# Kernel optimization log

Hardware: AMD Instinct MI355X
Metric: run time of the kernel (lower is better)

## Reference

```python
import jax, jax.numpy as jnp
import numpy as np

DIM = 384
WH, WW = 7, 7
N_HEADS = 12
HEAD_DIM = DIM // N_HEADS
SCALE = HEAD_DIM ** -0.5


def _relative_position_index(Wh, Ww):
    coords = np.stack(np.meshgrid(np.arange(Wh), np.arange(Ww), indexing='ij'))  # (2,Wh,Ww)
    cf = coords.reshape(2, -1)                       # (2, N)
    rc = cf[:, :, None] - cf[:, None, :]             # (2, N, N)
    rc = rc.transpose(1, 2, 0).copy()                # (N, N, 2)
    rc[..., 0] += Wh - 1
    rc[..., 1] += Ww - 1
    rc[..., 0] *= 2 * Ww - 1
    return jnp.asarray(rc.sum(-1))                   # (N, N) int

REL_IDX = _relative_position_index(WH, WW)


def setup_inputs() -> dict:
    key = jax.random.key(0)
    ks = jax.random.split(key, 5)
    B_, N, C = 4096, WH * WW, DIM
    nW = 64
    x = jax.random.normal(ks[0], (B_, N, C), dtype=jnp.float32)
    mask = jnp.zeros((nW, N, N), dtype=jnp.float32)  # 0/-inf additive mask; zeros = no shift
    qkv_w = jax.random.normal(ks[1], (3 * C, C), dtype=jnp.float32) * (C ** -0.5)
    qkv_b = jnp.zeros((3 * C,), dtype=jnp.float32)
    proj_w = jax.random.normal(ks[2], (C, C), dtype=jnp.float32) * (C ** -0.5)
    proj_b = jnp.zeros((C,), dtype=jnp.float32)
    rpb_table = jax.random.normal(ks[3], ((2 * WH - 1) * (2 * WW - 1), N_HEADS), dtype=jnp.float32) * 0.02
    return {"x": x, "mask": mask, "qkv_w": qkv_w, "qkv_b": qkv_b,
            "proj_w": proj_w, "proj_b": proj_b, "rpb_table": rpb_table}


def reference(x, mask, qkv_w, qkv_b, proj_w, proj_b, rpb_table):
    B_, N, C = x.shape
    H, hd = N_HEADS, HEAD_DIM
    # qkv projection -> (3, B_, H, N, hd)
    qkv = (x @ qkv_w.T + qkv_b).reshape(B_, N, 3, H, hd).transpose(2, 0, 3, 1, 4)
    q, k, v = qkv[0] * SCALE, qkv[1], qkv[2]
    attn = jnp.einsum('bhnd,bhmd->bhnm', q, k)                       # (B_, H, N, N)
    rpb = rpb_table[REL_IDX.reshape(-1)].reshape(N, N, H).transpose(2, 0, 1)  # (H, N, N)
    attn = attn + rpb[None]
    nW = mask.shape[0]
    attn = attn.reshape(B_ // nW, nW, H, N, N) + mask[None, :, None]
    attn = attn.reshape(B_, H, N, N)
    attn = jax.nn.softmax(attn, axis=-1)
    out = jnp.einsum('bhnm,bhmd->bhnd', attn, v)                     # (B_, H, N, hd)
    out = out.transpose(0, 2, 1, 3).reshape(B_, N, C)
    return out @ proj_w.T + proj_b
```

## Files before the change

### kernel.cpp

```cpp
#include <hip/hip_runtime.h>
#include <stdint.h>


typedef unsigned short u16;
typedef short short8 __attribute__((ext_vector_type(8)));
typedef float f32x4 __attribute__((ext_vector_type(4)));

static __device__ __forceinline__ u16 f2bf(float f) {
  unsigned u = __builtin_bit_cast(unsigned, f);
  return (u16)((u + 0x7fffu + ((u >> 16) & 1u)) >> 16);
}

static __device__ __forceinline__ void async_cp16(const u16* g, u16* l) {
  __builtin_amdgcn_global_load_lds(
      (__attribute__((address_space(1))) unsigned int*)g,
      (__attribute__((address_space(3))) unsigned int*)l, 16, 0, 0);
}

__global__ __launch_bounds__(256) void prep_kernel(
    const float* __restrict__ x, const float* __restrict__ wq,
    const float* __restrict__ wp, const float* __restrict__ rpt,
    u16* __restrict__ xb, u16* __restrict__ wqb, u16* __restrict__ wpb,
    float* __restrict__ rpbf)
{
  const int bid = blockIdx.x, tid = threadIdx.x;
  if (bid < 1024) {
    const float4* x4 = (const float4*)x;
    ushort4* o4 = (ushort4*)xb;
    for (unsigned i = bid * 256u + tid; i < 19267584u; i += 262144u) {
      float4 v = x4[i];
      ushort4 o; o.x = f2bf(v.x); o.y = f2bf(v.y); o.z = f2bf(v.z); o.w = f2bf(v.w);
      o4[i] = o;
    }
  } else if (bid < 1088) {
    for (unsigned i = (bid - 1024) * 256u + tid; i < 147456u; i += 16384u) {
      if (i < 110592u) {
        float4 v = ((const float4*)wq)[i];
        ushort4 o; o.x = f2bf(v.x); o.y = f2bf(v.y); o.z = f2bf(v.z); o.w = f2bf(v.w);
        ((ushort4*)wqb)[i] = o;
      } else {
        unsigned k = i - 110592u;
        float4 v = ((const float4*)wp)[k];
        ushort4 o; o.x = f2bf(v.x); o.y = f2bf(v.y); o.z = f2bf(v.z); o.w = f2bf(v.w);
        ((ushort4*)wpb)[k] = o;
      }
    }
  } else {
    for (int e = (bid - 1088) * 256 + tid; e < 28812; e += 2048) {
      int h = e / 2401, r2 = e - h * 2401;
      int i = r2 / 49, j = r2 - (r2 / 49) * 49;
      int rel = (i / 7 - j / 7 + 6) * 13 + (i % 7 - j % 7 + 6);
      rpbf[e] = rpt[rel * 12 + h];
    }
  }
}

template <int MODE>
__global__ __launch_bounds__(256) void gemm_nt(
    const u16* __restrict__ A, const u16* __restrict__ Bw,
    const float* __restrict__ bias, void* __restrict__ Cp, int Ntot)
{
  __shared__ u16 As[128 * 32];
  __shared__ u16 Bs[128 * 32];
  const int tid = threadIdx.x;
  const int wave = tid >> 6, lane = tid & 63;
  const int lr = lane & 15, quad = lane >> 4;
  const int m0 = blockIdx.y * 128, n0 = blockIdx.x * 128;
  const int wm = (wave & 1) * 64, wn = (wave >> 1) * 64;

  const int e0 = tid * 8;
  const int row0 = e0 >> 5, col0 = e0 & 31;

  f32x4 acc[4][4] = {};
  for (int k0 = 0; k0 < 384; k0 += 32) {
    __syncthreads();
    async_cp16(&A[(size_t)(m0 + row0) * 384 + k0 + col0],      As + wave * 512);
    async_cp16(&A[(size_t)(m0 + 64 + row0) * 384 + k0 + col0], As + 2048 + wave * 512);
    async_cp16(&Bw[(size_t)(n0 + row0) * 384 + k0 + col0],      Bs + wave * 512);
    async_cp16(&Bw[(size_t)(n0 + 64 + row0) * 384 + k0 + col0], Bs + 2048 + wave * 512);
    __syncthreads();

    short8 af[4], bf[4];
#pragma unroll
    for (int mi = 0; mi < 4; ++mi)
      af[mi] = *(const short8*)&As[(wm + mi * 16 + lr) * 32 + quad * 8];
#pragma unroll
    for (int ni = 0; ni < 4; ++ni)
      bf[ni] = *(const short8*)&Bs[(wn + ni * 16 + lr) * 32 + quad * 8];
#pragma unroll
    for (int mi = 0; mi < 4; ++mi)
#pragma unroll
      for (int ni = 0; ni < 4; ++ni)
        acc[mi][ni] = __builtin_amdgcn_mfma_f32_16x16x32_bf16(af[mi], bf[ni], acc[mi][ni], 0, 0, 0);
  }

  float bv[4];
#pragma unroll
  for (int ni = 0; ni < 4; ++ni) bv[ni] = bias[n0 + wn + ni * 16 + lr];
#pragma unroll
  for (int mi = 0; mi < 4; ++mi)
#pragma unroll
    for (int ni = 0; ni < 4; ++ni) {
      const int gcol = n0 + wn + ni * 16 + lr;
#pragma unroll
      for (int r = 0; r < 4; ++r) {
        const size_t grow = (size_t)(m0 + wm + mi * 16 + quad * 4 + r);
        float v = acc[mi][ni][r] + bv[ni];
        if (MODE == 0) {
          if (gcol < 384) v *= 0.17677669529663687f;
          ((u16*)Cp)[grow * Ntot + gcol] = f2bf(v);
        } else {
          ((float*)Cp)[grow * Ntot + gcol] = v;
        }
      }
    }
}

__global__ __launch_bounds__(256) void attn_kernel(
    const u16* __restrict__ qkv, const float* __restrict__ mask,
    const float* __restrict__ rpbf, u16* __restrict__ attnout)
{
  __shared__ u16 P_lds[4][64 * 64];
  __shared__ u16 VT_lds[4][32 * 64];
  const int tid = threadIdx.x;
  const int wave = tid >> 6, lane = tid & 63;
  const int lr = lane & 15, quad = lane >> 4;
  const int b = blockIdx.x / 3;
  const int h = (blockIdx.x - b * 3) * 4 + wave;

  const size_t base = (size_t)b * (49 * 1152);
  u16* P  = P_lds[wave];
  u16* Vt = VT_lds[wave];
  const short8 z8 = {0, 0, 0, 0, 0, 0, 0, 0};

  {
    const int dh = lane & 3;
    const int tk0 = lane >> 2;
#pragma unroll
    for (int p = 0; p < 4; ++p) {
      const int tok = p * 16 + tk0;
      short8 v = z8;
      if (tok < 49)
        v = *(const short8*)&qkv[base + (size_t)tok * 1152 + 768 + h * 32 + dh * 8];
#pragma unroll
      for (int j = 0; j < 8; ++j) {
        const int d = dh * 8 + j;
        Vt[d * 64 + (((tok >> 3) ^ j) * 8) + (tok & 7)] = ((const u16*)&v)[j];
      }
    }
  }

  short8 qf[4], kf[4];
#pragma unroll
  for (int mi = 0; mi < 4; ++mi) {
    const int row = mi * 16 + lr;
    qf[mi] = (row < 49)
        ? *(const short8*)&qkv[base + (size_t)row * 1152 + h * 32 + quad * 8] : z8;
  }
#pragma unroll
  for (int ni = 0; ni < 4; ++ni) {
    const int tok = ni * 16 + lr;
    kf[ni] = (tok < 49)
        ? *(const short8*)&qkv[base + (size_t)tok * 1152 + 384 + h * 32 + quad * 8] : z8;
  }
  f32x4 s[4][4] = {};
#pragma unroll
  for (int mi = 0; mi < 4; ++mi)
#pragma unroll
    for (int ni = 0; ni < 4; ++ni)
      s[mi][ni] = __builtin_amdgcn_mfma_f32_16x16x32_bf16(qf[mi], kf[ni], s[mi][ni], 0, 0, 0);

  const float* rh = &rpbf[h * 2401];
  const float* mw = &mask[(size_t)(b & 63) * 2401];
  float linv[4][4];
#pragma unroll
  for (int mi = 0; mi < 4; ++mi) {
#pragma unroll
    for (int r = 0; r < 4; ++r) {
      const int row = mi * 16 + quad * 4 + r;
      float vals[4];
#pragma unroll
      for (int ni = 0; ni < 4; ++ni) {
        const int col = ni * 16 + lr;
        float v;
        if (row < 49 && col < 49)
          v = s[mi][ni][r] + rh[row * 49 + col] + mw[row * 49 + col];
        else
          v = -1e30f;
        vals[ni] = v;
      }
      float m = fmaxf(fmaxf(vals[0], vals[1]), fmaxf(vals[2], vals[3]));
      m = fmaxf(m, __shfl_xor(m, 1));
      m = fmaxf(m, __shfl_xor(m, 2));
      m = fmaxf(m, __shfl_xor(m, 4));
      m = fmaxf(m, __shfl_xor(m, 8));
      float l = 0.f;
#pragma unroll
      for (int ni = 0; ni < 4; ++ni) {
        const float p = __expf(vals[ni] - m);
        l += p;
        const int col = ni * 16 + lr;
        P[row * 64 + (((col >> 3) ^ (row & 7)) * 8) + (col & 7)] = f2bf(p);
      }
      l += __shfl_xor(l, 1);
      l += __shfl_xor(l, 2);
      l += __shfl_xor(l, 4);
      l += __shfl_xor(l, 8);
      linv[mi][r] = 1.0f / l;
    }
  }

  f32x4 o[4][2] = {};
#pragma unroll
  for (int kh = 0; kh < 2; ++kh) {
    const int chunk = (kh * 4 + quad) ^ (lr & 7);
    short8 vf[2];
#pragma unroll
    for (int ni = 0; ni < 2; ++ni)
      vf[ni] = *(const short8*)&Vt[(ni * 16 + lr) * 64 + chunk * 8];
#pragma unroll
    for (int mi = 0; mi < 4; ++mi) {
      short8 pf = *(const short8*)&P[(mi * 16 + lr) * 64 + chunk * 8];
#pragma unroll
      for (int ni = 0; ni < 2; ++ni)
        o[mi][ni] = __builtin_amdgcn_mfma_f32_16x16x32_bf16(pf, vf[ni], o[mi][ni], 0, 0, 0);
    }
  }

  u16* outp = attnout + (size_t)b * (49 * 384) + h * 32;
#pragma unroll
  for (int mi = 0; mi < 4; ++mi)
#pragma unroll
    for (int r = 0; r < 4; ++r) {
      const int row = mi * 16 + quad * 4 + r;
      if (row < 49) {
        const float li = linv[mi][r];
#pragma unroll
        for (int ni = 0; ni < 2; ++ni)
          outp[row * 384 + ni * 16 + lr] = f2bf(o[mi][ni][r] * li);
      }
    }
}

extern "C" void kernel_launch(void* const* d_in, const int* in_sizes, int n_in,
                              void* d_out, int out_size, void* d_ws, size_t ws_size,
                              hipStream_t stream) {
  const float* x      = (const float*)d_in[0];
  const float* mask   = (const float*)d_in[1];
  const float* qkv_w  = (const float*)d_in[2];
  const float* qkv_b  = (const float*)d_in[3];
  const float* proj_w = (const float*)d_in[4];
  const float* proj_b = (const float*)d_in[5];
  const float* rpb_t  = (const float*)d_in[6];
  float* out = (float*)d_out;

  char* ws = (char*)d_ws;
  u16* qkv    = (u16*)ws;
  u16* xb     = (u16*)(ws + 462422016u);
  u16* attnout = xb;
  u16* wqb    = (u16*)(ws + 462422016u + 154140672u);
  u16* wpb    = wqb + 442368;
  float* rpbf = (float*)((char*)wpb + 294912u);

  prep_kernel<<<1096, 256, 0, stream>>>(x, qkv_w, proj_w, rpb_t, xb, wqb, wpb, rpbf);
  gemm_nt<0><<<dim3(9, 1568), 256, 0, stream>>>(xb, wqb, qkv_b, (void*)qkv, 1152);
  attn_kernel<<<12288, 256, 0, stream>>>(qkv, mask, rpbf, attnout);
  gemm_nt<1><<<dim3(3, 1568), 256, 0, stream>>>(attnout, wpb, proj_b, (void*)out, 384);
}
```

Measured before the change: 1.186 ms.

## Double-buffer GEMM LDS loads, swizzle LDS, stage coalesced epilogue, remap blocks per XCD

The GEMM kernel now double-buffers its LDS tiles, prefetching the next K-slice with async global-to-LDS copies while MFMAs run on the current one, which removes one barrier per iteration. LDS reads and writes use an XOR swizzle to avoid bank conflicts. The epilogue stages results through LDS so each thread issues 16-byte coalesced global stores instead of scattered scalar ones. The 2D grid becomes a 1D grid remapped so consecutive tiles land on the same XCD, and attention blocks get the same remap, to improve L2 locality. The cost is twice the LDS per block, which may reduce occupancy.

Result: no change. 1.166 ms (-1.7%).

```diff
diff --git a/kernel.cpp b/kernel.cpp
--- a/kernel.cpp
+++ b/kernel.cpp
@@ -58,62 +58,131 @@
 template <int MODE>
 __global__ __launch_bounds__(256) void gemm_nt(
     const u16* __restrict__ A, const u16* __restrict__ Bw,
-    const float* __restrict__ bias, void* __restrict__ Cp, int Ntot)
+    const float* __restrict__ bias, void* __restrict__ Cp)
 {
-  __shared__ u16 As[128 * 32];
-  __shared__ u16 Bs[128 * 32];
+  constexpr int NTOT = (MODE == 0) ? 1152 : 384;
+  constexpr int NX = NTOT / 128;
+  constexpr int CPX = (NX * 1568) / 8;
+  __shared__ u16 smem[16384];
+
   const int tid = threadIdx.x;
   const int wave = tid >> 6, lane = tid & 63;
   const int lr = lane & 15, quad = lane >> 4;
-  const int m0 = blockIdx.y * 128, n0 = blockIdx.x * 128;
+
+  const int lid = (blockIdx.x & 7) * CPX + (blockIdx.x >> 3);
+  const int by = lid / NX;
+  const int bx = lid - by * NX;
+  const int m0 = by * 128, n0 = bx * 128;
   const int wm = (wave & 1) * 64, wn = (wave >> 1) * 64;
 
-  const int e0 = tid * 8;
-  const int row0 = e0 >> 5, col0 = e0 & 31;
+  const int r4 = tid >> 2;
+  const int cs = ((tid & 3) ^ ((r4 >> 1) & 3)) * 8;
+  const size_t ga0 = (size_t)(m0 + r4) * 384 + cs;
+  const size_t ga1 = (size_t)(m0 + 64 + r4) * 384 + cs;
+  const size_t gb0 = (size_t)(n0 + r4) * 384 + cs;
+  const size_t gb1 = (size_t)(n0 + 64 + r4) * 384 + cs;
 
   f32x4 acc[4][4] = {};
-  for (int k0 = 0; k0 < 384; k0 += 32) {
-    __syncthreads();
-    async_cp16(&A[(size_t)(m0 + row0) * 384 + k0 + col0],      As + wave * 512);
-    async_cp16(&A[(size_t)(m0 + 64 + row0) * 384 + k0 + col0], As + 2048 + wave * 512);
-    async_cp16(&Bw[(size_t)(n0 + row0) * 384 + k0 + col0],      Bs + wave * 512);
-    async_cp16(&Bw[(size_t)(n0 + 64 + row0) * 384 + k0 + col0], Bs + 2048 + wave * 512);
-    __syncthreads();
-
+  const int sw = (lr >> 1) & 3;
+
+  {
+    u16* As = smem; u16* Bs = smem + 4096;
+    async_cp16(&A[ga0], As + wave * 512);
+    async_cp16(&A[ga1], As + 2048 + wave * 512);
+    async_cp16(&Bw[gb0], Bs + wave * 512);
+    async_cp16(&Bw[gb1], Bs + 2048 + wave * 512);
+  }
+  __syncthreads();
+
+  int buf = 0;
+#pragma unroll 2
+  for (int it = 0; it < 12; ++it) {
+    u16* As = smem + buf * 8192;
+    u16* Bs = As + 4096;
+    if (it < 11) {
+      u16* An = smem + (buf ^ 1) * 8192;
+      u16* Bn = An + 4096;
+      const int k0 = (it + 1) * 32;
+      async_cp16(&A[ga0 + k0], An + wave * 512);
+      async_cp16(&A[ga1 + k0], An + 2048 + wave * 512);
+      async_cp16(&Bw[gb0 + k0], Bn + wave * 512);
+      async_cp16(&Bw[gb1 + k0], Bn + 2048 + wave * 512);
+    }
     short8 af[4], bf[4];
 #pragma unroll
     for (int mi = 0; mi < 4; ++mi)
-      af[mi] = *(const short8*)&As[(wm + mi * 16 + lr) * 32 + quad * 8];
+      af[mi] = *(const short8*)&As[(wm + mi * 16 + lr) * 32 + ((quad ^ sw) * 8)];
 #pragma unroll
     for (int ni = 0; ni < 4; ++ni)
-      bf[ni] = *(const short8*)&Bs[(wn + ni * 16 + lr) * 32 + quad * 8];
+      bf[ni] = *(const short8*)&Bs[(wn + ni * 16 + lr) * 32 + ((quad ^ sw) * 8)];
 #pragma unroll
     for (int mi = 0; mi < 4; ++mi)
 #pragma unroll
       for (int ni = 0; ni < 4; ++ni)
         acc[mi][ni] = __builtin_amdgcn_mfma_f32_16x16x32_bf16(af[mi], bf[ni], acc[mi][ni], 0, 0, 0);
+    __syncthreads();
+    buf ^= 1;
   }
 
   float bv[4];
 #pragma unroll
   for (int ni = 0; ni < 4; ++ni) bv[ni] = bias[n0 + wn + ni * 16 + lr];
-#pragma unroll
-  for (int mi = 0; mi < 4; ++mi)
-#pragma unroll
-    for (int ni = 0; ni < 4; ++ni) {
-      const int gcol = n0 + wn + ni * 16 + lr;
-#pragma unroll
-      for (int r = 0; r < 4; ++r) {
-        const size_t grow = (size_t)(m0 + wm + mi * 16 + quad * 4 + r);
-        float v = acc[mi][ni][r] + bv[ni];
-        if (MODE == 0) {
-          if (gcol < 384) v *= 0.17677669529663687f;
-          ((u16*)Cp)[grow * Ntot + gcol] = f2bf(v);
-        } else {
-          ((float*)Cp)[grow * Ntot + gcol] = v;
+
+  if (MODE == 0) {
+    const float sc = (n0 < 384) ? 0.17677669529663687f : 1.0f;
+    u16* ot = smem;
+#pragma unroll
+    for (int mi = 0; mi < 4; ++mi)
+#pragma unroll
+      for (int ni = 0; ni < 4; ++ni)
+#pragma unroll
+        for (int r = 0; r < 4; ++r) {
+          const int row = wm + mi * 16 + quad * 4 + r;
+          const int col = wn + ni * 16 + lr;
+          const int slot = (col >> 3) ^ ((row >> 2) & 7);
+          ot[row * 128 + slot * 8 + (col & 7)] =
+              f2bf((acc[mi][ni][r] + bv[ni]) * sc);
         }
-      }
-    }
+    __syncthreads();
+    u16* outp = (u16*)Cp;
+#pragma unroll
+    for (int j = 0; j < 8; ++j) {
+      const int cid = j * 256 + tid;
+      const int row = cid >> 4, slot = cid & 15;
+      const int c8 = slot ^ ((row >> 2) & 7);
+      *(short8*)&outp[(size_t)(m0 + row) * NTOT + n0 + c8 * 8] =
+          *(const short8*)&ot[row * 128 + slot * 8];
+    }
+  } else {
+    float* fl = (float*)smem;
+    float* outp = (float*)Cp;
+#pragma unroll
+    for (int h = 0; h < 2; ++h) {
+      if ((wave & 1) == h) {
+#pragma unroll
+        for (int mi = 0; mi < 4; ++mi)
+#pragma unroll
+          for (int ni = 0; ni < 4; ++ni)
+#pragma unroll
+            for (int r = 0; r < 4; ++r) {
+              const int lrow = mi * 16 + quad * 4 + r;
+              const int col = wn + ni * 16 + lr;
+              const int slot = (col >> 2) ^ ((lrow >> 2) & 7);
+              fl[lrow * 128 + slot * 4 + (col & 3)] = acc[mi][ni][r] + bv[ni];
+            }
+      }
+      __syncthreads();
+#pragma unroll
+      for (int j = 0; j < 8; ++j) {
+        const int cid = j * 256 + tid;
+        const int lrow = cid >> 5, slot = cid & 31;
+        const int c4 = slot ^ ((lrow >> 2) & 7);
+        *(f32x4*)&outp[(size_t)(m0 + h * 64 + lrow) * NTOT + n0 + c4 * 4] =
+            *(const f32x4*)&fl[lrow * 128 + slot * 4];
+      }
+      if (h == 0) __syncthreads();
+    }
+  }
 }
 
 __global__ __launch_bounds__(256) void attn_kernel(
@@ -125,8 +194,9 @@
   const int tid = threadIdx.x;
   const int wave = tid >> 6, lane = tid & 63;
   const int lr = lane & 15, quad = lane >> 4;
-  const int b = blockIdx.x / 3;
-  const int h = (blockIdx.x - b * 3) * 4 + wave;
+  const int bl = (blockIdx.x & 7) * 1536 + (blockIdx.x >> 3);
+  const int b = bl / 3;
+  const int h = (bl - b * 3) * 4 + wave;
 
   const size_t base = (size_t)b * (49 * 1152);
   u16* P  = P_lds[wave];
@@ -263,7 +333,7 @@
   float* rpbf = (float*)((char*)wpb + 294912u);
 
   prep_kernel<<<1096, 256, 0, stream>>>(x, qkv_w, proj_w, rpb_t, xb, wqb, wpb, rpbf);
-  gemm_nt<0><<<dim3(9, 1568), 256, 0, stream>>>(xb, wqb, qkv_b, (void*)qkv, 1152);
+  gemm_nt<0><<<14112, 256, 0, stream>>>(xb, wqb, qkv_b, (void*)qkv);
   attn_kernel<<<12288, 256, 0, stream>>>(qkv, mask, rpbf, attnout);
-  gemm_nt<1><<<dim3(3, 1568), 256, 0, stream>>>(attnout, wpb, proj_b, (void*)out, 384);
-}
+  gemm_nt<1><<<4704, 256, 0, stream>>>(attnout, wpb, proj_b, (void*)out);
+}
```
